# Kernel optimization log

Measured on AMD Instinct MI355X. Metric: run time of the kernel, lower is better.

Reference implementation:

```python
import jax, jax.numpy as jnp
import numpy as np
from jax import lax

TEMPERATURE = 30.0
PAD = 1  # padding init-kwarg; stride=1, dilation=1


def setup_inputs() -> dict:
    key = jax.random.key(0)
    ks = jax.random.split(key, 8)
    B, D, HID, NF, K, CIN, COUT, HW = 32, 512, 256, 8, 3, 64, 64, 64
    return {
        "filter_condition_input": jax.random.normal(ks[0], (B, D), jnp.float32),
        "model_input": jax.random.normal(ks[1], (B, CIN, HW, HW), jnp.float32),
        "fc1_w": jax.random.normal(ks[2], (HID, D), jnp.float32) * (2.0 / D) ** 0.5,
        "fc1_b": jnp.zeros((HID,), jnp.float32),
        "fc2_w": jax.random.normal(ks[3], (NF, HID), jnp.float32) * (2.0 / HID) ** 0.5,
        "fc2_b": jnp.zeros((NF,), jnp.float32),
        "weight": jax.random.normal(ks[4], (NF, COUT, CIN, K, K), jnp.float32) * 0.05,
        "bias_p": jax.random.normal(ks[5], (NF, COUT), jnp.float32) * 0.05,
    }


def reference(filter_condition_input, model_input, fc1_w, fc1_b, fc2_w, fc2_b, weight, bias_p):
    # Routing MLP -> softmax attention over the num_filters kernel bank
    h = jax.nn.relu(filter_condition_input @ fc1_w.T + fc1_b)
    logits = h @ fc2_w.T + fc2_b
    attn = jax.nn.softmax(logits / TEMPERATURE, axis=1)  # [B, NF]

    # Per-sample aggregated conv kernels and biases
    agg_w = jnp.einsum("bf,foikl->boikl", attn, weight)  # [B, O, Cin, K, K]
    agg_b = attn @ bias_p                                  # [B, O]

    # groups = batch_size grouped conv == independent per-sample conv (vmapped)
    def conv1(x_i, w_i):  # x_i: [Cin,H,W], w_i: [O,Cin,K,K]
        return lax.conv_general_dilated(
            x_i[None], w_i, window_strides=(1, 1),
            padding=((PAD, PAD), (PAD, PAD)),
            dimension_numbers=("NCHW", "OIHW", "NCHW"))[0]

    out = jax.vmap(conv1)(model_input, agg_w) + agg_b[:, :, None, None]  # [B,O,H,W]
    return out, attn
```

## Files before the change

### kernel.cpp

```cpp
#include <hip/hip_runtime.h>
#include <hip/hip_bf16.h>

typedef __hip_bfloat16 bf16;
typedef unsigned short u16;
typedef unsigned int   u32;

#define B_    32
#define D_    512
#define HID_  256
#define NF_   8
#define CIN_  64
#define COUT_ 64
#define HW_   64
#define CONV_OUT_ELEMS (B_ * COUT_ * HW_ * HW_)
#define WBANK_ (NF_ * 36864)

typedef __attribute__((ext_vector_type(8))) short  short8;
typedef __attribute__((ext_vector_type(4))) float  floatx4;

__device__ inline float b2f(bf16 v) { return __bfloat162float(v); }
__device__ inline bf16  f2b(float f) { return __float2bfloat16(f); }
__device__ inline u16 f2bu(float f) { union { bf16 h; u16 u; } c; c.h = __float2bfloat16(f); return c.u; }
__device__ inline float bu2f(u16 u) { union { u32 i; float f; } c; c.i = ((u32)u) << 16; return c.f; }

__device__ inline float ldf(const void* p, int i, int isbf) {
    return isbf ? __bfloat162float(((const bf16*)p)[i]) : ((const float*)p)[i];
}

__device__ inline int word_bf16_sane(u32 v) {
    u32 lo = v & 0xFFFFu;
    u32 ex = (lo >> 7) & 0xFFu;
    return (lo == 0u || (ex >= 64u && ex <= 191u)) ? 1 : 0;
}

__global__ __launch_bounds__(256) void fc1_kernel(
    const void* __restrict__ x,
    const void* __restrict__ fc1_w,
    const void* __restrict__ fc1_b,
    float* __restrict__ ws_hs)
{
    const int h = blockIdx.x;
    const int t = threadIdx.x;
    const int b = t >> 3, seg = t & 7;
    __shared__ int fl[3];
    if (t < 3) fl[t] = 1;
    __syncthreads();
    if (t < 96) {
        const int g = t >> 5, k = t & 31;
        const void* buf = (g == 0) ? x : (g == 1) ? fc1_w : fc1_b;
        const int elems = (g == 0) ? B_ * D_ : (g == 1) ? HID_ * D_ : HID_;
        const int nw = elems >> 1;
        const int n = nw < 32 ? nw : 32;
        if (k < n && nw >= 1) {
            u32 v = ((const u32*)buf)[k * (nw / n)];
            if (!word_bf16_sane(v)) atomicAnd(&fl[g], 0);
        }
    }
    __syncthreads();
    const int xbf = fl[0], wbf = fl[1], b1bf = fl[2];

    const int xoff = b * D_ + seg * 64;
    const int woff = h * D_ + seg * 64;
    float p = 0.f;
    if (!xbf && !wbf) {
        float4 xr[16], wr[16];
        const float4* xp = (const float4*)((const float*)x + xoff);
        const float4* wp = (const float4*)((const float*)fc1_w + woff);
#pragma unroll
        for (int c = 0; c < 16; ++c) xr[c] = xp[c];
#pragma unroll
        for (int c = 0; c < 16; ++c) wr[c] = wp[c];
#pragma unroll
        for (int c = 0; c < 16; ++c)
            p += xr[c].x * wr[c].x + xr[c].y * wr[c].y + xr[c].z * wr[c].z + xr[c].w * wr[c].w;
    } else if (xbf && wbf) {
        uint4 xr[8], wr[8];
        const uint4* xp = (const uint4*)((const bf16*)x + xoff);
        const uint4* wp = (const uint4*)((const bf16*)fc1_w + woff);
#pragma unroll
        for (int c = 0; c < 8; ++c) xr[c] = xp[c];
#pragma unroll
        for (int c = 0; c < 8; ++c) wr[c] = wp[c];
#pragma unroll
        for (int c = 0; c < 8; ++c) {
            const u32 xw[4] = { xr[c].x, xr[c].y, xr[c].z, xr[c].w };
            const u32 ww[4] = { wr[c].x, wr[c].y, wr[c].z, wr[c].w };
#pragma unroll
            for (int q2 = 0; q2 < 4; ++q2)
                p += bu2f((u16)(xw[q2] & 0xFFFF)) * bu2f((u16)(ww[q2] & 0xFFFF))
                   + bu2f((u16)(xw[q2] >> 16))    * bu2f((u16)(ww[q2] >> 16));
        }
    } else {
        for (int c = 0; c < 64; ++c) p += ldf(x, xoff + c, xbf) * ldf(fc1_w, woff + c, wbf);
    }
    p += __shfl_xor(p, 1);
    p += __shfl_xor(p, 2);
    p += __shfl_xor(p, 4);
    if (seg == 0) {
        p += ldf(fc1_b, h, b1bf);
        ws_hs[b * HID_ + h] = p > 0.f ? p : 0.f;
    }
}

__global__ __launch_bounds__(256) void fc2_kernel(
    const void* __restrict__ fc2_w,
    const void* __restrict__ fc2_b,
    const void* __restrict__ bias_p,
    const void* __restrict__ xin,
    const float* __restrict__ ws_hs,
    float* __restrict__ ws_attn, float* __restrict__ ws_aggb,
    void* __restrict__ d_out)
{
    __shared__ float hs[HID_];
    __shared__ float at[NF_];
    __shared__ int fl[4];
    const int b = blockIdx.x, t = threadIdx.x;
    if (t < 4) fl[t] = 1;
    hs[t] = ws_hs[b * HID_ + t];
    __syncthreads();
    if (t < 128) {
        const int g = t >> 5, k = t & 31;
        const void* buf = (g == 0) ? fc2_w : (g == 1) ? fc2_b : (g == 2) ? bias_p : xin;
        const int elems = (g == 0) ? NF_ * HID_ : (g == 1) ? NF_ : (g == 2) ? NF_ * COUT_
                                                : B_ * CIN_ * HW_ * HW_;
        const int nw = elems >> 1;
        const int n = nw < 32 ? nw : 32;
        if (k < n && nw >= 1) {
            u32 v = ((const u32*)buf)[k * (nw / n)];
            if (!word_bf16_sane(v)) atomicAnd(&fl[g], 0);
        }
    }
    __syncthreads();
    const int w2bf = fl[0], b2bf = fl[1], bpbf = fl[2], obf = fl[3];

    const int f = t >> 5, j = t & 31;
    const float* hp = hs + j * 8;
    float p;
    if (w2bf) {
        uint4 u = *(const uint4*)((const bf16*)fc2_w + f * HID_ + j * 8);
        p = bu2f((u16)(u.x & 0xFFFF)) * hp[0] + bu2f((u16)(u.x >> 16)) * hp[1]
          + bu2f((u16)(u.y & 0xFFFF)) * hp[2] + bu2f((u16)(u.y >> 16)) * hp[3]
          + bu2f((u16)(u.z & 0xFFFF)) * hp[4] + bu2f((u16)(u.z >> 16)) * hp[5]
          + bu2f((u16)(u.w & 0xFFFF)) * hp[6] + bu2f((u16)(u.w >> 16)) * hp[7];
    } else {
        const float* r = (const float*)fc2_w + f * HID_ + j * 8;
        float4 a = *(const float4*)r, c = *(const float4*)(r + 4);
        p = a.x * hp[0] + a.y * hp[1] + a.z * hp[2] + a.w * hp[3]
          + c.x * hp[4] + c.y * hp[5] + c.z * hp[6] + c.w * hp[7];
    }
#pragma unroll
    for (int m = 16; m; m >>= 1) p += __shfl_xor(p, m);
    if (j == 0) at[f] = (p + ldf(fc2_b, f, b2bf)) * (1.0f / 30.0f);
    __syncthreads();

    if (t == 0) {
        float m = at[0];
#pragma unroll
        for (int ff = 1; ff < NF_; ++ff) m = fmaxf(m, at[ff]);
        float e[NF_], ssum = 0.f;
#pragma unroll
        for (int ff = 0; ff < NF_; ++ff) { e[ff] = __expf(at[ff] - m); ssum += e[ff]; }
        float inv = 1.0f / ssum;
#pragma unroll
        for (int ff = 0; ff < NF_; ++ff) at[ff] = e[ff] * inv;
    }
    __syncthreads();
    if (t < NF_) {
        ws_attn[b * NF_ + t] = at[t];
        if (obf) ((bf16*)d_out)[CONV_OUT_ELEMS + b * NF_ + t] = f2b(at[t]);
        else    ((float*)d_out)[CONV_OUT_ELEMS + b * NF_ + t] = at[t];
    }
    if (t < COUT_) {
        float s = 0.f;
#pragma unroll
        for (int ff = 0; ff < NF_; ++ff) s += at[ff] * ldf(bias_p, ff * COUT_ + t, bpbf);
        ws_aggb[b * COUT_ + t] = s;
    }
}

__global__ __launch_bounds__(256) void agg_kernel(
    const void* __restrict__ weight,
    const float* __restrict__ ws_attn,
    u16* __restrict__ aggw)
{
    __shared__ float lds[2304];
    __shared__ float s_at[NF_];
    __shared__ int   s_wbf;
    const int t  = threadIdx.x;
    const int b  = blockIdx.x >> 4;
    const int o0 = (blockIdx.x & 15) * 4;

    if (t == 0) s_wbf = 1;
    if (t < NF_) s_at[t] = ws_attn[b * NF_ + t];
    __syncthreads();
    if (t < 32) {
        const int nw = WBANK_ >> 1, step = nw / 32;
        u32 v = ((const u32*)weight)[t * step];
        if (!word_bf16_sane(v)) atomicAnd(&s_wbf, 0);
    }
    __syncthreads();
    const int wbf = s_wbf;

#pragma unroll
    for (int j = 0; j < 9; ++j) {
        const int flat = t + 256 * j;
        const int o_l = flat / 576, rr = flat - o_l * 576;
        const int gbase = (o0 + o_l) * 576 + rr;
        float s = 0.f;
        if (wbf) {
#pragma unroll
            for (int f = 0; f < NF_; ++f) s += s_at[f] * b2f(((const bf16*)weight)[f * 36864 + gbase]);
        } else {
#pragma unroll
            for (int f = 0; f < NF_; ++f) s += s_at[f] * ((const float*)weight)[f * 36864 + gbase];
        }
        lds[flat] = s;
    }
    __syncthreads();
#pragma unroll
    for (int j = 0; j < 9; ++j) {
        const int e = t + 256 * j;
        const int tap = e >> 8, o_l = (e >> 6) & 3, ci = e & 63;
        aggw[b * 36864 + tap * 4096 + (o0 + o_l) * 64 + ci] = f2bu(lds[o_l * 576 + ci * 9 + tap]);
    }
}

__global__ __launch_bounds__(256, 2) void conv_mfma(
    const void* __restrict__ xin,
    const u16*  __restrict__ aggw,
    const float* __restrict__ aggb,
    void* __restrict__ out)
{
    __shared__ __align__(16) u16 smem[31104];
    __shared__ float bias_s[COUT_];
    __shared__ int s_ok;
    u16* in_s = smem;
    u16* w_s  = smem + 12672;

    const int t    = threadIdx.x;
    const int bz   = blockIdx.x;
    const int b    = bz >> 4;
    const int y0   = (bz & 15) * 4;
    const int wv   = t >> 6;
    const int lane = t & 63, l15 = lane & 15, q = lane >> 4;

    if (t == 0) s_ok = 1;
    __syncthreads();
    if (t < 32) {
        u32 w = ((const u32*)xin)[t * 131072];
        if (!word_bf16_sane(w)) atomicAnd(&s_ok, 0);
    }
    if (t < COUT_) bias_s[t] = aggb[b * COUT_ + t];
    __syncthreads();
    const int inbf = s_ok;

    floatx4 acc[4][4];
#pragma unroll
    for (int mt = 0; mt < 4; ++mt)
#pragma unroll
        for (int nt = 0; nt < 4; ++nt) acc[mt][nt] = (floatx4)0.f;

    for (int ph = 0; ph < 2; ++ph) {
        const int ci0 = ph * 32;
        __syncthreads();
#pragma unroll
        for (int j = 0; j < 9; ++j) {
            const int item = t + 256 * j;
            const int o = item & 63, cib = (item >> 6) & 3, tap = item >> 8;
            uint4 v = *(const uint4*)(aggw + b * 36864 + tap * 4096 + o * 64 + ci0 + cib * 8);
            *(uint4*)&w_s[((tap * 4 + cib) * 64 + o) * 8] = v;
        }
#pragma unroll
        for (int j = 0; j < 3; ++j) {
            const int item = t + 256 * j;
            const int cp = item & 15, z = item >> 4;
            const int r = z % 6, ch = z / 6;
            const int gy = y0 - 1 + r, gx0 = ch * 8;
            const int ci = ci0 + cp * 2;
            union { uint4 v; u16 s[8]; } a0, a1;
            if (gy >= 0 && gy < HW_) {
                const int gi = ((b * CIN_ + ci) * HW_ + gy) * HW_ + gx0;
                if (inbf) {
                    a0.v = *(const uint4*)((const bf16*)xin + gi);
                    a1.v = *(const uint4*)((const bf16*)xin + gi + HW_ * HW_);
                } else {
                    const float* p0 = (const float*)xin + gi;
                    const float* p1 = p0 + HW_ * HW_;
                    float4 f00 = *(const float4*)p0, f01 = *(const float4*)(p0 + 4);
                    float4 f10 = *(const float4*)p1, f11 = *(const float4*)(p1 + 4);
                    a0.s[0]=f2bu(f00.x); a0.s[1]=f2bu(f00.y); a0.s[2]=f2bu(f00.z); a0.s[3]=f2bu(f00.w);
                    a0.s[4]=f2bu(f01.x); a0.s[5]=f2bu(f01.y); a0.s[6]=f2bu(f01.z); a0.s[7]=f2bu(f01.w);
                    a1.s[0]=f2bu(f10.x); a1.s[1]=f2bu(f10.y); a1.s[2]=f2bu(f10.z); a1.s[3]=f2bu(f10.w);
                    a1.s[4]=f2bu(f11.x); a1.s[5]=f2bu(f11.y); a1.s[6]=f2bu(f11.z); a1.s[7]=f2bu(f11.w);
                }
            } else {
                a0.v = make_uint4(0,0,0,0); a1.v = make_uint4(0,0,0,0);
            }
            const int cib = cp >> 2, p = cp & 3;
            u32* dst = (u32*)in_s;
#pragma unroll
            for (int k = 0; k < 8; ++k) {
                const int col = 1 + gx0 + k;
                dst[((r * 4 + cib) * 66 + col) * 4 + p] = (u32)a0.s[k] | ((u32)a1.s[k] << 16);
            }
        }
        if (t < 192) {
            const int cp = t & 15, z = t >> 4;
            const int r = z % 6, col = (z / 6) ? 65 : 0;
            ((u32*)in_s)[((r * 4 + (cp >> 2)) * 66 + col) * 4 + (cp & 3)] = 0u;
        }
        __syncthreads();
#pragma unroll
        for (int tap = 0; tap < 9; ++tap) {
            const int kh = tap / 3, kw = tap % 3;
            short8 af[4], bfr[4];
#pragma unroll
            for (int mt = 0; mt < 4; ++mt)
                af[mt] = *(const short8*)&w_s[((tap * 4 + q) * 64 + mt * 16 + l15) * 8];
#pragma unroll
            for (int nt = 0; nt < 4; ++nt)
                bfr[nt] = *(const short8*)&in_s[(((wv + kh) * 4 + q) * 66 + nt * 16 + l15 + kw) * 8];
#pragma unroll
            for (int mt = 0; mt < 4; ++mt)
#pragma unroll
                for (int nt = 0; nt < 4; ++nt)
                    acc[mt][nt] = __builtin_amdgcn_mfma_f32_16x16x32_bf16(af[mt], bfr[nt], acc[mt][nt], 0, 0, 0);
        }
    }

    __syncthreads();
    u16* out_s = smem;
#pragma unroll
    for (int mt = 0; mt < 4; ++mt) {
        floatx4 bb = *(const floatx4*)&bias_s[mt * 16 + q * 4];
#pragma unroll
        for (int nt = 0; nt < 4; ++nt) {
#pragma unroll
            for (int rg = 0; rg < 4; ++rg) {
                const float v = acc[mt][nt][rg] + bb[rg];
                out_s[(wv * 64 + (mt * 16 + q * 4 + rg)) * 68 + nt * 16 + l15] = f2bu(v);
            }
        }
    }
    __syncthreads();
    const int outbf = inbf;
#pragma unroll
    for (int j = 0; j < 16; ++j) {
        const int c = t + 256 * j;
        const int x0 = (c & 15) * 4, o = (c >> 4) & 63, w2 = c >> 10;
        const u16* src = &out_s[(w2 * 64 + o) * 68 + x0];
        const u16 h0 = src[0], h1 = src[1], h2 = src[2], h3 = src[3];
        const int gidx = ((b * COUT_ + o) * HW_ + (y0 + w2)) * HW_ + x0;
        if (outbf) {
            uint2 pk; pk.x = (u32)h0 | ((u32)h1 << 16); pk.y = (u32)h2 | ((u32)h3 << 16);
            *(uint2*)((u16*)out + gidx) = pk;
        } else {
            float4 f; f.x = bu2f(h0); f.y = bu2f(h1); f.z = bu2f(h2); f.w = bu2f(h3);
            *(float4*)((float*)out + gidx) = f;
        }
    }
}

extern "C" void kernel_launch(void* const* d_in, const int* in_sizes, int n_in,
                              void* d_out, int out_size, void* d_ws, size_t ws_size,
                              hipStream_t stream) {
    const void* x      = d_in[0];
    const void* xin    = d_in[1];
    const void* fc1_w  = d_in[2];
    const void* fc1_b  = d_in[3];
    const void* fc2_w  = d_in[4];
    const void* fc2_b  = d_in[5];
    const void* weight = d_in[6];
    const void* bias_p = d_in[7];

    float* ws      = (float*)d_ws;
    float* ws_attn = ws;
    float* ws_aggb = ws + 256;
    float* ws_hs   = ws + 2304;
    u16*   ws_aggw = (u16*)(ws + 10496);

    fc1_kernel<<<dim3(HID_), dim3(256), 0, stream>>>(x, fc1_w, fc1_b, ws_hs);

    fc2_kernel<<<dim3(B_), dim3(256), 0, stream>>>(
        fc2_w, fc2_b, bias_p, xin, ws_hs, ws_attn, ws_aggb, d_out);

    agg_kernel<<<dim3(B_ * 16), dim3(256), 0, stream>>>(weight, ws_attn, ws_aggw);

    conv_mfma<<<dim3(B_ * 16), dim3(256), 0, stream>>>(xin, ws_aggw, ws_aggb, d_out);
}
```

Measured before the change: 130.3 us.

## Pre-transpose input to NHWC bf16 and read conv operands directly from global

Adds a prep pass, merged into the fc1 kernel launch, that converts the NCHW input to an NHWC bf16 buffer in workspace. The conv kernel then loads MFMA fragments for weights and input straight from global memory (relying on cache) instead of staging them in shared memory, which removes the LDS staging loops and the barriers between them. The cost is an extra full read and write of the input, plus many uncoalesced-ish global fragment loads with edge branches in the inner loop. The occupancy hint of 2 blocks per CU is also dropped.

```diff
diff --git a/kernel.cpp b/kernel.cpp
--- a/kernel.cpp
+++ b/kernel.cpp
@@ -33,16 +33,68 @@
     return (lo == 0u || (ex >= 64u && ex <= 191u)) ? 1 : 0;
 }
 
-__global__ __launch_bounds__(256) void fc1_kernel(
+__global__ __launch_bounds__(256) void prep_kernel(
+    const void* __restrict__ xin,
     const void* __restrict__ x,
     const void* __restrict__ fc1_w,
     const void* __restrict__ fc1_b,
+    u16* __restrict__ xin_t,
     float* __restrict__ ws_hs)
 {
-    const int h = blockIdx.x;
+    __shared__ u16 tr[64][66];
+    __shared__ int fl[4];
+    const int blk = blockIdx.x;
     const int t = threadIdx.x;
+
+    if (blk < 2048) {
+        const int b = blk >> 6, y = blk & 63;
+        if (t == 0) fl[0] = 1;
+        __syncthreads();
+        if (t < 32) {
+            u32 w = ((const u32*)xin)[t * 131072];
+            if (!word_bf16_sane(w)) atomicAnd(&fl[0], 0);
+        }
+        __syncthreads();
+        const int inbf = fl[0];
+
+        const int ci = t >> 2, xq = (t & 3) * 16;
+        u16 vals[16];
+        if (inbf) {
+            const bf16* src = (const bf16*)xin + (((b * CIN_ + ci) * HW_ + y) * HW_ + xq);
+            uint4 v0 = *(const uint4*)src;
+            uint4 v1 = *(const uint4*)(src + 8);
+            const u32 w8[8] = { v0.x, v0.y, v0.z, v0.w, v1.x, v1.y, v1.z, v1.w };
+#pragma unroll
+            for (int k = 0; k < 8; ++k) {
+                vals[2 * k]     = (u16)(w8[k] & 0xFFFF);
+                vals[2 * k + 1] = (u16)(w8[k] >> 16);
+            }
+        } else {
+            const float* src = (const float*)xin + (((b * CIN_ + ci) * HW_ + y) * HW_ + xq);
+#pragma unroll
+            for (int c = 0; c < 4; ++c) {
+                float4 f = *(const float4*)(src + c * 4);
+                vals[c * 4 + 0] = f2bu(f.x); vals[c * 4 + 1] = f2bu(f.y);
+                vals[c * 4 + 2] = f2bu(f.z); vals[c * 4 + 3] = f2bu(f.w);
+            }
+        }
+#pragma unroll
+        for (int k = 0; k < 16; ++k) tr[xq + k][ci] = vals[k];
+        __syncthreads();
+
+        const int px = t >> 2, cg = (t & 3) * 16;
+        u32 wd[8];
+#pragma unroll
+        for (int w = 0; w < 8; ++w)
+            wd[w] = (u32)tr[px][cg + 2 * w] | ((u32)tr[px][cg + 2 * w + 1] << 16);
+        u16* dst = xin_t + (((b * HW_ + y) * HW_ + px) * CIN_ + cg);
+        ((uint4*)dst)[0] = make_uint4(wd[0], wd[1], wd[2], wd[3]);
+        ((uint4*)dst)[1] = make_uint4(wd[4], wd[5], wd[6], wd[7]);
+        return;
+    }
+
+    const int h = blk - 2048;
     const int b = t >> 3, seg = t & 7;
-    __shared__ int fl[3];
     if (t < 3) fl[t] = 1;
     __syncthreads();
     if (t < 96) {
@@ -225,17 +277,16 @@
     }
 }
 
-__global__ __launch_bounds__(256, 2) void conv_mfma(
-    const void* __restrict__ xin,
+__global__ __launch_bounds__(256) void conv_mfma2(
+    const u16*  __restrict__ xin_t,
     const u16*  __restrict__ aggw,
     const float* __restrict__ aggb,
+    const void* __restrict__ xin,
     void* __restrict__ out)
 {
-    __shared__ __align__(16) u16 smem[31104];
+    __shared__ u16 out_s[4 * 64 * 68];
     __shared__ float bias_s[COUT_];
     __shared__ int s_ok;
-    u16* in_s = smem;
-    u16* w_s  = smem + 12672;
 
     const int t    = threadIdx.x;
     const int bz   = blockIdx.x;
@@ -252,7 +303,7 @@
     }
     if (t < COUT_) bias_s[t] = aggb[b * COUT_ + t];
     __syncthreads();
-    const int inbf = s_ok;
+    const int outbf = s_ok;
 
     floatx4 acc[4][4];
 #pragma unroll
@@ -260,76 +311,43 @@
 #pragma unroll
         for (int nt = 0; nt < 4; ++nt) acc[mt][nt] = (floatx4)0.f;
 
-    for (int ph = 0; ph < 2; ++ph) {
-        const int ci0 = ph * 32;
-        __syncthreads();
-#pragma unroll
-        for (int j = 0; j < 9; ++j) {
-            const int item = t + 256 * j;
-            const int o = item & 63, cib = (item >> 6) & 3, tap = item >> 8;
-            uint4 v = *(const uint4*)(aggw + b * 36864 + tap * 4096 + o * 64 + ci0 + cib * 8);
-            *(uint4*)&w_s[((tap * 4 + cib) * 64 + o) * 8] = v;
-        }
-#pragma unroll
-        for (int j = 0; j < 3; ++j) {
-            const int item = t + 256 * j;
-            const int cp = item & 15, z = item >> 4;
-            const int r = z % 6, ch = z / 6;
-            const int gy = y0 - 1 + r, gx0 = ch * 8;
-            const int ci = ci0 + cp * 2;
-            union { uint4 v; u16 s[8]; } a0, a1;
-            if (gy >= 0 && gy < HW_) {
-                const int gi = ((b * CIN_ + ci) * HW_ + gy) * HW_ + gx0;
-                if (inbf) {
-                    a0.v = *(const uint4*)((const bf16*)xin + gi);
-                    a1.v = *(const uint4*)((const bf16*)xin + gi + HW_ * HW_);
-                } else {
-                    const float* p0 = (const float*)xin + gi;
-                    const float* p1 = p0 + HW_ * HW_;
-                    float4 f00 = *(const float4*)p0, f01 = *(const float4*)(p0 + 4);
-                    float4 f10 = *(const float4*)p1, f11 = *(const float4*)(p1 + 4);
-                    a0.s[0]=f2bu(f00.x); a0.s[1]=f2bu(f00.y); a0.s[2]=f2bu(f00.z); a0.s[3]=f2bu(f00.w);
-                    a0.s[4]=f2bu(f01.x); a0.s[5]=f2bu(f01.y); a0.s[6]=f2bu(f01.z); a0.s[7]=f2bu(f01.w);
-                    a1.s[0]=f2bu(f10.x); a1.s[1]=f2bu(f10.y); a1.s[2]=f2bu(f10.z); a1.s[3]=f2bu(f10.w);
-                    a1.s[4]=f2bu(f11.x); a1.s[5]=f2bu(f11.y); a1.s[6]=f2bu(f11.z); a1.s[7]=f2bu(f11.w);
+    const u16* Abase = aggw + b * 36864;
+    const int laneA = l15 * 64 + q * 8;
+    const int laneB = l15 * 64 + q * 8;
+
+#pragma unroll
+    for (int kh = 0; kh < 3; ++kh) {
+        const int gy = y0 + wv + kh - 1;
+        if (gy >= 0 && gy < HW_) {
+            const u16* Brow = xin_t + (b * HW_ + gy) * (HW_ * CIN_);
+#pragma unroll
+            for (int kw = 0; kw < 3; ++kw) {
+                const u16* Atap = Abase + (kh * 3 + kw) * 4096;
+#pragma unroll
+                for (int ks = 0; ks < 2; ++ks) {
+                    short8 af[4], bf[4];
+#pragma unroll
+                    for (int mt = 0; mt < 4; ++mt)
+                        af[mt] = *(const short8*)(Atap + mt * 1024 + ks * 32 + laneA);
+#pragma unroll
+                    for (int nt = 0; nt < 4; ++nt) {
+                        const int col = nt * 16 + l15 + kw - 1;
+                        if (col >= 0 && col < HW_)
+                            bf[nt] = *(const short8*)(Brow + col * 64 + ks * 32 + q * 8);
+                        else
+                            bf[nt] = (short8)0;
+                    }
+#pragma unroll
+                    for (int mt = 0; mt < 4; ++mt)
+#pragma unroll
+                        for (int nt = 0; nt < 4; ++nt)
+                            acc[mt][nt] = __builtin_amdgcn_mfma_f32_16x16x32_bf16(
+                                af[mt], bf[nt], acc[mt][nt], 0, 0, 0);
                 }
-            } else {
-                a0.v = make_uint4(0,0,0,0); a1.v = make_uint4(0,0,0,0);
             }
-            const int cib = cp >> 2, p = cp & 3;
-            u32* dst = (u32*)in_s;
-#pragma unroll
-            for (int k = 0; k < 8; ++k) {
-                const int col = 1 + gx0 + k;
-                dst[((r * 4 + cib) * 66 + col) * 4 + p] = (u32)a0.s[k] | ((u32)a1.s[k] << 16);
-            }
-        }
-        if (t < 192) {
-            const int cp = t & 15, z = t >> 4;
-            const int r = z % 6, col = (z / 6) ? 65 : 0;
-            ((u32*)in_s)[((r * 4 + (cp >> 2)) * 66 + col) * 4 + (cp & 3)] = 0u;
-        }
-        __syncthreads();
-#pragma unroll
-        for (int tap = 0; tap < 9; ++tap) {
-            const int kh = tap / 3, kw = tap % 3;
-            short8 af[4], bfr[4];
-#pragma unroll
-            for (int mt = 0; mt < 4; ++mt)
-                af[mt] = *(const short8*)&w_s[((tap * 4 + q) * 64 + mt * 16 + l15) * 8];
-#pragma unroll
-            for (int nt = 0; nt < 4; ++nt)
-                bfr[nt] = *(const short8*)&in_s[(((wv + kh) * 4 + q) * 66 + nt * 16 + l15 + kw) * 8];
-#pragma unroll
-            for (int mt = 0; mt < 4; ++mt)
-#pragma unroll
-                for (int nt = 0; nt < 4; ++nt)
-                    acc[mt][nt] = __builtin_amdgcn_mfma_f32_16x16x32_bf16(af[mt], bfr[nt], acc[mt][nt], 0, 0, 0);
-        }
-    }
-
-    __syncthreads();
-    u16* out_s = smem;
+        }
+    }
+
 #pragma unroll
     for (int mt = 0; mt < 4; ++mt) {
         floatx4 bb = *(const floatx4*)&bias_s[mt * 16 + q * 4];
@@ -343,7 +361,6 @@
         }
     }
     __syncthreads();
-    const int outbf = inbf;
 #pragma unroll
     for (int j = 0; j < 16; ++j) {
         const int c = t + 256 * j;
@@ -378,13 +395,16 @@
     float* ws_aggb = ws + 256;
     float* ws_hs   = ws + 2304;
     u16*   ws_aggw = (u16*)(ws + 10496);
-
-    fc1_kernel<<<dim3(HID_), dim3(256), 0, stream>>>(x, fc1_w, fc1_b, ws_hs);
+    u16*   ws_xint = (u16*)(ws + 600320);
+
+    prep_kernel<<<dim3(2048 + HID_), dim3(256), 0, stream>>>(
+        xin, x, fc1_w, fc1_b, ws_xint, ws_hs);
 
     fc2_kernel<<<dim3(B_), dim3(256), 0, stream>>>(
         fc2_w, fc2_b, bias_p, xin, ws_hs, ws_attn, ws_aggb, d_out);
 
     agg_kernel<<<dim3(B_ * 16), dim3(256), 0, stream>>>(weight, ws_attn, ws_aggw);
 
-    conv_mfma<<<dim3(B_ * 16), dim3(256), 0, stream>>>(xin, ws_aggw, ws_aggb, d_out);
-}
+    conv_mfma2<<<dim3(B_ * 16), dim3(256), 0, stream>>>(
+        ws_xint, ws_aggw, ws_aggb, xin, d_out);
+}
```

After: 157.2 us. 20.6% more time.
